# Performance work log

Hardware: AMD Instinct MI355X
Metric: run time of the kernel (lower is better)

The kernel has to match this reference:

```python
import jax, jax.numpy as jnp
import numpy as np

KH, KW = 3, 3
C_OUT = 32


def setup_inputs() -> dict:
    key = jax.random.key(0)
    k1, k2, k3 = jax.random.split(key, 3)
    B, H, W, C_IN = 32, 128, 128, 32
    P_DIM = 128
    X = jax.random.normal(k1, (B, H, W, C_IN), dtype=jnp.float32)
    P = jax.random.normal(k2, (B, P_DIM), dtype=jnp.float32)
    # hypernetwork Dense weight: p_dim -> kh*kw*c_in*c_out (no bias, no activation)
    dense_w = jax.random.normal(k3, (P_DIM, KH * KW * C_IN * C_OUT), dtype=jnp.float32) * 0.05
    return {"X": X, "P": P, "dense_w": dense_w}


def _conv_one(x, w):
    # x: [H, W, c_in], w: [kh, kw, c_in, c_out] -> [H, W, c_out], SAME padding, stride 1
    y = jax.lax.conv_general_dilated(
        x[None], w, window_strides=(1, 1), padding="SAME",
        dimension_numbers=("NHWC", "HWIO", "NHWC"))
    return y[0]


def reference(X, P, dense_w):
    B = X.shape[0]
    c_in = X.shape[-1]
    # hypernetwork: per-sample conv kernels
    A = P @ dense_w                              # [B, kh*kw*c_in*c_out]
    Wk = A.reshape(B, KH, KW, c_in, C_OUT)       # [B, kh, kw, c_in, c_out]
    # batched per-sample conv (equivalent to tf.map_fn over conv2d)
    return jax.vmap(_conv_one)(X, Wk)            # [B, H, W, c_out]
```

## Files before the change

### kernel.cpp

```cpp
#include <hip/hip_runtime.h>


#define BATCH 32
#define HDIM 128
#define WDIM 128
#define CIN 32
#define COUT 32
#define PDIM 128
#define KCOLS 9216

typedef _Float16 f16x8 __attribute__((ext_vector_type(8)));
typedef float f32x4 __attribute__((ext_vector_type(4)));

__device__ __forceinline__ f16x8 zero8() {
    f16x8 z;
#pragma unroll
    for (int j = 0; j < 8; ++j) z[j] = (_Float16)0.f;
    return z;
}

__device__ __forceinline__ f16x8 cvt8(f32x4 lo, f32x4 hi) {
    f16x8 o;
#pragma unroll
    for (int j = 0; j < 4; ++j) {
        o[j] = (_Float16)lo[j];
        o[4 + j] = (_Float16)hi[j];
    }
    return o;
}

__global__ __launch_bounds__(256) void hyper_gemm(const float* __restrict__ P,
                                                  const float* __restrict__ Dw,
                                                  unsigned short* __restrict__ WB) {
    const int tid = threadIdx.x;
    const int lane = tid & 63;
    const int cg = blockIdx.x % 144;
    const int bq = blockIdx.x / 144;
    const int col = cg * 64 + lane;
    const int b0 = __builtin_amdgcn_readfirstlane(bq * 16 + (tid >> 6) * 4);
    const float* pb = P + (size_t)b0 * PDIM;

    float acc[4];
#pragma unroll
    for (int j = 0; j < 4; ++j) acc[j] = 0.f;

#pragma unroll 2
    for (int mm = 0; mm < PDIM; mm += 16) {
        float d[16];
#pragma unroll
        for (int u = 0; u < 16; ++u) d[u] = Dw[(size_t)(mm + u) * KCOLS + col];
#pragma unroll
        for (int u = 0; u < 16; ++u) {
#pragma unroll
            for (int j = 0; j < 4; ++j) acc[j] += d[u] * pb[j * PDIM + mm + u];
        }
    }

    const int co = col & 31;
    const int k = col >> 5;
    const int kc = k >> 5;
    const int ci = k & 31;
    const int base =
        ((kc * 2 + (co >> 4)) * 64 + (ci >> 3) * 16 + (co & 15)) * 8 + (ci & 7);
#pragma unroll
    for (int j = 0; j < 4; ++j) {
        _Float16 v = (_Float16)acc[j];
        WB[(size_t)(b0 + j) * KCOLS + base] = __builtin_bit_cast(unsigned short, v);
    }
}

__device__ __forceinline__ f16x8 halo_ld(const f32x4* __restrict__ gp, int px) {
    const bool ok = (unsigned)px < 128u;
    const int p = ok ? px : 0;
    f32x4 lo = gp[p * 8];
    f32x4 hi = gp[p * 8 + 1];
    f16x8 o = cvt8(lo, hi);
    if (!ok) o = zero8();
    return o;
}

__global__ __launch_bounds__(256, 3) void conv_s4(const float* __restrict__ X,
                                                  const unsigned short* __restrict__ WB,
                                                  float* __restrict__ Y) {
    __shared__ f16x8 Xs[4 * 512];
    __shared__ f16x8 BFs[KCOLS / 8];
    const int tid = threadIdx.x;

    const int wg = blockIdx.x;
    const int id = (wg & 7) * 128 + (wg >> 3);
    const int b = id >> 5;
    const int hg = id & 31;
    const int r0 = hg * 4;

    const int wave = tid >> 6;
    const int lane = tid & 63;
    const int q = lane >> 4;
    const int m16 = lane & 15;

    {
        const f16x8* wbp = (const f16x8*)(WB + (size_t)b * KCOLS);
#pragma unroll
        for (int i = 0; i < 5; ++i) {
            const int idx = tid + i * 256;
            if (idx < KCOLS / 8) BFs[idx] = wbp[idx];
        }
    }

    {
        const int px_s = tid >> 1;
        const int qb = (tid & 1) * 2;
#pragma unroll
        for (int r = 0; r < 4; ++r) {
#pragma unroll
            for (int p = 0; p < 2; ++p) {
                const int q_s = qb + p;
                const float* src =
                    X + (((size_t)b * HDIM + r0 + r) * WDIM + px_s) * CIN + q_s * 8;
                f32x4 lo = *(const f32x4*)src;
                f32x4 hi = *(const f32x4*)(src + 4);
                const int g_s = px_s * 4 + ((q_s ^ (px_s >> 1)) & 3);
                Xs[r * 512 + g_s] = cvt8(lo, hi);
            }
        }
    }
    __syncthreads();

    const bool top = (wave == 0);
    const bool bot = (wave == 3);
    const bool gvalid = top ? (hg != 0) : (bot ? (hg != 31) : false);
    const int grow = top ? (hg ? r0 - 1 : 0) : (r0 + 4);
    const f32x4* gp = (const f32x4*)X +
                      ((size_t)b * HDIM + (gvalid ? grow : 0)) * (WDIM * CIN / 4) +
                      q * 2;

    f16x8 hal[3];
    if (gvalid) {
#pragma unroll
        for (int kw = 0; kw < 3; ++kw) hal[kw] = halo_ld(gp, m16 + kw - 1);
    } else {
#pragma unroll
        for (int kw = 0; kw < 3; ++kw) hal[kw] = zero8();
    }

    int va[3];
#pragma unroll
    for (int kw = 0; kw < 3; ++kw) {
        const int px = m16 + kw - 1;
        const int sl = (q ^ (px >> 1)) & 3;
        va[kw] = (wave - 1) * 8192 + px * 64 + sl * 16;
    }

    const char* xsb = (const char*)Xs;
    const f16x8* bfl = BFs + lane;
    const int h = r0 + wave;
    float* ybase = Y + (((size_t)b * HDIM + h) * WDIM + q * 4) * COUT + m16;

#pragma unroll
    for (int t = 0; t < 8; ++t) {
        f32x4 acc0 = {0.f, 0.f, 0.f, 0.f};
        f32x4 acc1 = {0.f, 0.f, 0.f, 0.f};

#pragma unroll
        for (int kh = 0; kh < 3; ++kh) {
            f16x8 a0, a1, a2;
            const bool use_lds =
                (kh == 1) || (kh == 0 && wave != 0) || (kh == 2 && wave != 3);
            if (use_lds) {
                int v0 = va[0] + kh * 8192;
                int v1 = va[1] + kh * 8192;
                int v2 = va[2] + kh * 8192;
                if (t == 0) v0 += (m16 == 0) ? 64 : 0;
                if (t == 7) v2 -= (m16 == 15) ? 64 : 0;
                a0 = *(const f16x8*)(xsb + v0);
                a1 = *(const f16x8*)(xsb + v1);
                a2 = *(const f16x8*)(xsb + v2);
                if (t == 0 && m16 == 0) a0 = zero8();
                if (t == 7 && m16 == 15) a2 = zero8();
            } else {
                a0 = hal[0];
                a1 = hal[1];
                a2 = hal[2];
                if (gvalid && t < 7) {
#pragma unroll
                    for (int kw = 0; kw < 3; ++kw)
                        hal[kw] = halo_ld(gp, (t + 1) * 16 + m16 + kw - 1);
                }
            }
            acc0 = __builtin_amdgcn_mfma_f32_16x16x32_f16(a0, bfl[((kh * 3 + 0) * 2 + 0) * 64], acc0, 0, 0, 0);
            acc1 = __builtin_amdgcn_mfma_f32_16x16x32_f16(a0, bfl[((kh * 3 + 0) * 2 + 1) * 64], acc1, 0, 0, 0);
            acc0 = __builtin_amdgcn_mfma_f32_16x16x32_f16(a1, bfl[((kh * 3 + 1) * 2 + 0) * 64], acc0, 0, 0, 0);
            acc1 = __builtin_amdgcn_mfma_f32_16x16x32_f16(a1, bfl[((kh * 3 + 1) * 2 + 1) * 64], acc1, 0, 0, 0);
            acc0 = __builtin_amdgcn_mfma_f32_16x16x32_f16(a2, bfl[((kh * 3 + 2) * 2 + 0) * 64], acc0, 0, 0, 0);
            acc1 = __builtin_amdgcn_mfma_f32_16x16x32_f16(a2, bfl[((kh * 3 + 2) * 2 + 1) * 64], acc1, 0, 0, 0);
        }

        float* yp = ybase + t * 16 * COUT;
#pragma unroll
        for (int r = 0; r < 4; ++r) {
            yp[r * COUT] = acc0[r];
            yp[r * COUT + 16] = acc1[r];
        }

#pragma unroll
        for (int kw = 0; kw < 3; ++kw) va[kw] += 1024;
    }
}

extern "C" void kernel_launch(void* const* d_in, const int* in_sizes, int n_in,
                              void* d_out, int out_size, void* d_ws, size_t ws_size,
                              hipStream_t stream) {
    const float* X = (const float*)d_in[0];
    const float* P = (const float*)d_in[1];
    const float* Dw = (const float*)d_in[2];
    float* Y = (float*)d_out;
    (void)ws_size;

    unsigned short* WB = (unsigned short*)d_ws;

    hipLaunchKernelGGL(hyper_gemm, dim3(288), dim3(256), 0, stream, P, Dw, WB);
    hipLaunchKernelGGL(conv_s4, dim3(1024), dim3(256), 0, stream, X, WB, Y);
}
```

Baseline: 146.7 us.

## Switch conv MFMA tiles from 16x16x32 to 32x32x16 with matching weight layout

Changes the per-wave conv tile from 16 pixels by 32 output channels, built from two 16x16x32 MFMAs, to a single 32x32x16 MFMA over 32 pixels and 32 output channels. The hypernetwork GEMM now writes weights in a layout that matches the new B-operand fragments, and the LDS and halo addressing are redone for 32-pixel tiles with two 8-channel halves. The aim is fewer MFMA issues and LDS B-fragment loads per output, at the cost of more live registers for halos and accumulators and a different store pattern.

Result: faster. 141.4 us (-3.6%).

```diff
diff --git a/kernel.cpp b/kernel.cpp
--- a/kernel.cpp
+++ b/kernel.cpp
@@ -11,6 +11,7 @@
 
 typedef _Float16 f16x8 __attribute__((ext_vector_type(8)));
 typedef float f32x4 __attribute__((ext_vector_type(4)));
+typedef float f32x16 __attribute__((ext_vector_type(16)));
 
 __device__ __forceinline__ f16x8 zero8() {
     f16x8 z;
@@ -61,7 +62,7 @@
     const int kc = k >> 5;
     const int ci = k & 31;
     const int base =
-        ((kc * 2 + (co >> 4)) * 64 + (ci >> 3) * 16 + (co & 15)) * 8 + (ci & 7);
+        ((kc * 2 + (ci >> 4)) * 64 + ((ci >> 3) & 1) * 32 + co) * 8 + (ci & 7);
 #pragma unroll
     for (int j = 0; j < 4; ++j) {
         _Float16 v = (_Float16)acc[j];
@@ -69,19 +70,20 @@
     }
 }
 
-__device__ __forceinline__ f16x8 halo_ld(const f32x4* __restrict__ gp, int px) {
+__device__ __forceinline__ f16x8 halo_ld32(const f32x4* __restrict__ gp, int px,
+                                           int oct) {
     const bool ok = (unsigned)px < 128u;
     const int p = ok ? px : 0;
-    f32x4 lo = gp[p * 8];
-    f32x4 hi = gp[p * 8 + 1];
+    f32x4 lo = gp[p * 8 + oct * 2];
+    f32x4 hi = gp[p * 8 + oct * 2 + 1];
     f16x8 o = cvt8(lo, hi);
     if (!ok) o = zero8();
     return o;
 }
 
-__global__ __launch_bounds__(256, 3) void conv_s4(const float* __restrict__ X,
-                                                  const unsigned short* __restrict__ WB,
-                                                  float* __restrict__ Y) {
+__global__ __launch_bounds__(256, 3) void conv_w32(const float* __restrict__ X,
+                                                   const unsigned short* __restrict__ WB,
+                                                   float* __restrict__ Y) {
     __shared__ f16x8 Xs[4 * 512];
     __shared__ f16x8 BFs[KCOLS / 8];
     const int tid = threadIdx.x;
@@ -94,8 +96,8 @@
 
     const int wave = tid >> 6;
     const int lane = tid & 63;
-    const int q = lane >> 4;
-    const int m16 = lane & 15;
+    const int m32 = lane & 31;
+    const int hi = lane >> 5;
 
     {
         const f16x8* wbp = (const f16x8*)(WB + (size_t)b * KCOLS);
@@ -117,9 +119,9 @@
                 const float* src =
                     X + (((size_t)b * HDIM + r0 + r) * WDIM + px_s) * CIN + q_s * 8;
                 f32x4 lo = *(const f32x4*)src;
-                f32x4 hi = *(const f32x4*)(src + 4);
+                f32x4 hi4 = *(const f32x4*)(src + 4);
                 const int g_s = px_s * 4 + ((q_s ^ (px_s >> 1)) & 3);
-                Xs[r * 512 + g_s] = cvt8(lo, hi);
+                Xs[r * 512 + g_s] = cvt8(lo, hi4);
             }
         }
     }
@@ -130,79 +132,98 @@
     const bool gvalid = top ? (hg != 0) : (bot ? (hg != 31) : false);
     const int grow = top ? (hg ? r0 - 1 : 0) : (r0 + 4);
     const f32x4* gp = (const f32x4*)X +
-                      ((size_t)b * HDIM + (gvalid ? grow : 0)) * (WDIM * CIN / 4) +
-                      q * 2;
-
-    f16x8 hal[3];
+                      ((size_t)b * HDIM + (gvalid ? grow : 0)) * (WDIM * CIN / 4);
+
+    f16x8 hal[3][2];
     if (gvalid) {
 #pragma unroll
-        for (int kw = 0; kw < 3; ++kw) hal[kw] = halo_ld(gp, m16 + kw - 1);
+        for (int kw = 0; kw < 3; ++kw)
+#pragma unroll
+            for (int h = 0; h < 2; ++h)
+                hal[kw][h] = halo_ld32(gp, m32 + kw - 1, 2 * h + hi);
     } else {
 #pragma unroll
-        for (int kw = 0; kw < 3; ++kw) hal[kw] = zero8();
-    }
-
-    int va[3];
-#pragma unroll
-    for (int kw = 0; kw < 3; ++kw) {
-        const int px = m16 + kw - 1;
-        const int sl = (q ^ (px >> 1)) & 3;
-        va[kw] = (wave - 1) * 8192 + px * 64 + sl * 16;
+        for (int kw = 0; kw < 3; ++kw)
+#pragma unroll
+            for (int h = 0; h < 2; ++h) hal[kw][h] = zero8();
+    }
+
+    int o0[2], o1[2], o2[2], o00[2];
+    {
+        const int p0 = m32 - 1, p1 = m32, p2 = m32 + 1;
+#pragma unroll
+        for (int h = 0; h < 2; ++h) {
+            const int s = 2 * h + hi;
+            o0[h] = p0 * 64 + ((s ^ ((p0 >> 1) & 3)) & 3) * 16;
+            o1[h] = p1 * 64 + ((s ^ ((p1 >> 1) & 3)) & 3) * 16;
+            o2[h] = p2 * 64 + ((s ^ ((p2 >> 1) & 3)) & 3) * 16;
+            const int pc = (m32 == 0) ? 0 : p0;
+            o00[h] = pc * 64 + ((s ^ ((pc >> 1) & 3)) & 3) * 16;
+        }
     }
 
     const char* xsb = (const char*)Xs;
     const f16x8* bfl = BFs + lane;
-    const int h = r0 + wave;
-    float* ybase = Y + (((size_t)b * HDIM + h) * WDIM + q * 4) * COUT + m16;
-
-#pragma unroll
-    for (int t = 0; t < 8; ++t) {
-        f32x4 acc0 = {0.f, 0.f, 0.f, 0.f};
-        f32x4 acc1 = {0.f, 0.f, 0.f, 0.f};
+    const int h_out = r0 + wave;
+    const int co = m32;
+    float* ybase = Y + (((size_t)b * HDIM + h_out) * WDIM) * COUT + co;
+
+#pragma unroll
+    for (int t = 0; t < 4; ++t) {
+        f32x16 acc = {};
 
 #pragma unroll
         for (int kh = 0; kh < 3; ++kh) {
-            f16x8 a0, a1, a2;
+            f16x8 a[3][2];
             const bool use_lds =
                 (kh == 1) || (kh == 0 && wave != 0) || (kh == 2 && wave != 3);
             if (use_lds) {
-                int v0 = va[0] + kh * 8192;
-                int v1 = va[1] + kh * 8192;
-                int v2 = va[2] + kh * 8192;
-                if (t == 0) v0 += (m16 == 0) ? 64 : 0;
-                if (t == 7) v2 -= (m16 == 15) ? 64 : 0;
-                a0 = *(const f16x8*)(xsb + v0);
-                a1 = *(const f16x8*)(xsb + v1);
-                a2 = *(const f16x8*)(xsb + v2);
-                if (t == 0 && m16 == 0) a0 = zero8();
-                if (t == 7 && m16 == 15) a2 = zero8();
+                const int ro = (wave - 1 + kh) * 8192;
+#pragma unroll
+                for (int h = 0; h < 2; ++h) {
+                    const int ad0 =
+                        ro + ((t == 0) ? o00[h] : (o0[h] + t * 2048));
+                    const int ad1 = ro + o1[h] + t * 2048;
+                    const int ad2 = ro + o2[h] + t * 2048 -
+                                    ((t == 3 && m32 == 31) ? 64 : 0);
+                    a[0][h] = *(const f16x8*)(xsb + ad0);
+                    a[1][h] = *(const f16x8*)(xsb + ad1);
+                    a[2][h] = *(const f16x8*)(xsb + ad2);
+                }
+                if (t == 0 && m32 == 0) { a[0][0] = zero8(); a[0][1] = zero8(); }
+                if (t == 3 && m32 == 31) { a[2][0] = zero8(); a[2][1] = zero8(); }
             } else {
-                a0 = hal[0];
-                a1 = hal[1];
-                a2 = hal[2];
-                if (gvalid && t < 7) {
+#pragma unroll
+                for (int kw = 0; kw < 3; ++kw)
+#pragma unroll
+                    for (int h = 0; h < 2; ++h) a[kw][h] = hal[kw][h];
+                if (gvalid && t < 3) {
 #pragma unroll
                     for (int kw = 0; kw < 3; ++kw)
-                        hal[kw] = halo_ld(gp, (t + 1) * 16 + m16 + kw - 1);
+#pragma unroll
+                        for (int h = 0; h < 2; ++h)
+                            hal[kw][h] = halo_ld32(gp, (t + 1) * 32 + m32 + kw - 1,
+                                                   2 * h + hi);
                 }
             }
-            acc0 = __builtin_amdgcn_mfma_f32_16x16x32_f16(a0, bfl[((kh * 3 + 0) * 2 + 0) * 64], acc0, 0, 0, 0);
-            acc1 = __builtin_amdgcn_mfma_f32_16x16x32_f16(a0, bfl[((kh * 3 + 0) * 2 + 1) * 64], acc1, 0, 0, 0);
-            acc0 = __builtin_amdgcn_mfma_f32_16x16x32_f16(a1, bfl[((kh * 3 + 1) * 2 + 0) * 64], acc0, 0, 0, 0);
-            acc1 = __builtin_amdgcn_mfma_f32_16x16x32_f16(a1, bfl[((kh * 3 + 1) * 2 + 1) * 64], acc1, 0, 0, 0);
-            acc0 = __builtin_amdgcn_mfma_f32_16x16x32_f16(a2, bfl[((kh * 3 + 2) * 2 + 0) * 64], acc0, 0, 0, 0);
-            acc1 = __builtin_amdgcn_mfma_f32_16x16x32_f16(a2, bfl[((kh * 3 + 2) * 2 + 1) * 64], acc1, 0, 0, 0);
-        }
-
-        float* yp = ybase + t * 16 * COUT;
-#pragma unroll
-        for (int r = 0; r < 4; ++r) {
-            yp[r * COUT] = acc0[r];
-            yp[r * COUT + 16] = acc1[r];
-        }
-
-#pragma unroll
-        for (int kw = 0; kw < 3; ++kw) va[kw] += 1024;
+#pragma unroll
+            for (int kw = 0; kw < 3; ++kw) {
+#pragma unroll
+                for (int h = 0; h < 2; ++h) {
+                    acc = __builtin_amdgcn_mfma_f32_32x32x16_f16(
+                        a[kw][h], bfl[(((kh * 3 + kw) * 2) + h) * 64], acc, 0, 0, 0);
+                }
+            }
+        }
+
+        float* yp = ybase + (size_t)(t * 32 + 4 * hi) * COUT;
+#pragma unroll
+        for (int r2 = 0; r2 < 4; ++r2) {
+#pragma unroll
+            for (int r1 = 0; r1 < 4; ++r1) {
+                yp[(size_t)(r1 + 8 * r2) * COUT] = acc[r2 * 4 + r1];
+            }
+        }
     }
 }
 
@@ -218,5 +239,5 @@
     unsigned short* WB = (unsigned short*)d_ws;
 
     hipLaunchKernelGGL(hyper_gemm, dim3(288), dim3(256), 0, stream, P, Dw, WB);
-    hipLaunchKernelGGL(conv_s4, dim3(1024), dim3(256), 0, stream, X, WB, Y);
-}
+    hipLaunchKernelGGL(conv_w32, dim3(1024), dim3(256), 0, stream, X, WB, Y);
+}
```

## Split conv work across 8 waves per block, two half-row waves per row

Applied to the files above, without the earlier changes.

Doubles the conv block to 512 threads, so each output row is handled by two waves that each cover half of the 8 column tiles. Staging loads are respread so each thread converts one 8-channel group per row. The aim is more waves in flight to hide LDS and global latency and to speed up the weight and input staging. The trade-off is more register and occupancy pressure under launch_bounds(512,8), and the halo loads for the top and bottom rows are now issued by two waves each.

Measured after the change: 139.7 us. -4.8%, faster.

```diff
diff --git a/kernel.cpp b/kernel.cpp
--- a/kernel.cpp
+++ b/kernel.cpp
@@ -79,9 +79,9 @@
     return o;
 }
 
-__global__ __launch_bounds__(256, 3) void conv_s4(const float* __restrict__ X,
-                                                  const unsigned short* __restrict__ WB,
-                                                  float* __restrict__ Y) {
+__global__ __launch_bounds__(512, 8) void conv_tlp(const float* __restrict__ X,
+                                                   const unsigned short* __restrict__ WB,
+                                                   float* __restrict__ Y) {
     __shared__ f16x8 Xs[4 * 512];
     __shared__ f16x8 BFs[KCOLS / 8];
     const int tid = threadIdx.x;
@@ -93,40 +93,35 @@
     const int r0 = hg * 4;
 
     const int wave = tid >> 6;
+    const int row = wave >> 1;
+    const int half = wave & 1;
     const int lane = tid & 63;
     const int q = lane >> 4;
     const int m16 = lane & 15;
+    const int t0 = half * 4;
 
     {
         const f16x8* wbp = (const f16x8*)(WB + (size_t)b * KCOLS);
-#pragma unroll
-        for (int i = 0; i < 5; ++i) {
-            const int idx = tid + i * 256;
-            if (idx < KCOLS / 8) BFs[idx] = wbp[idx];
-        }
+        for (int i = tid; i < KCOLS / 8; i += 512) BFs[i] = wbp[i];
     }
 
     {
-        const int px_s = tid >> 1;
-        const int qb = (tid & 1) * 2;
+        const int px_s = tid >> 2;
+        const int q_s = tid & 3;
+        const int g_s = px_s * 4 + ((q_s ^ (px_s >> 1)) & 3);
 #pragma unroll
         for (int r = 0; r < 4; ++r) {
-#pragma unroll
-            for (int p = 0; p < 2; ++p) {
-                const int q_s = qb + p;
-                const float* src =
-                    X + (((size_t)b * HDIM + r0 + r) * WDIM + px_s) * CIN + q_s * 8;
-                f32x4 lo = *(const f32x4*)src;
-                f32x4 hi = *(const f32x4*)(src + 4);
-                const int g_s = px_s * 4 + ((q_s ^ (px_s >> 1)) & 3);
-                Xs[r * 512 + g_s] = cvt8(lo, hi);
-            }
+            const float* src =
+                X + (((size_t)b * HDIM + r0 + r) * WDIM + px_s) * CIN + q_s * 8;
+            f32x4 lo = *(const f32x4*)src;
+            f32x4 hi = *(const f32x4*)(src + 4);
+            Xs[r * 512 + g_s] = cvt8(lo, hi);
         }
     }
     __syncthreads();
 
-    const bool top = (wave == 0);
-    const bool bot = (wave == 3);
+    const bool top = (row == 0);
+    const bool bot = (row == 3);
     const bool gvalid = top ? (hg != 0) : (bot ? (hg != 31) : false);
     const int grow = top ? (hg ? r0 - 1 : 0) : (r0 + 4);
     const f32x4* gp = (const f32x4*)X +
@@ -136,7 +131,8 @@
     f16x8 hal[3];
     if (gvalid) {
 #pragma unroll
-        for (int kw = 0; kw < 3; ++kw) hal[kw] = halo_ld(gp, m16 + kw - 1);
+        for (int kw = 0; kw < 3; ++kw)
+            hal[kw] = halo_ld(gp, t0 * 16 + m16 + kw - 1);
     } else {
 #pragma unroll
         for (int kw = 0; kw < 3; ++kw) hal[kw] = zero8();
@@ -145,18 +141,19 @@
     int va[3];
 #pragma unroll
     for (int kw = 0; kw < 3; ++kw) {
-        const int px = m16 + kw - 1;
+        const int px = t0 * 16 + m16 + kw - 1;
         const int sl = (q ^ (px >> 1)) & 3;
-        va[kw] = (wave - 1) * 8192 + px * 64 + sl * 16;
+        va[kw] = (row - 1) * 8192 + px * 64 + sl * 16;
     }
 
     const char* xsb = (const char*)Xs;
     const f16x8* bfl = BFs + lane;
-    const int h = r0 + wave;
+    const int h = r0 + row;
     float* ybase = Y + (((size_t)b * HDIM + h) * WDIM + q * 4) * COUT + m16;
 
 #pragma unroll
-    for (int t = 0; t < 8; ++t) {
+    for (int tt = 0; tt < 4; ++tt) {
+        const int t = t0 + tt;
         f32x4 acc0 = {0.f, 0.f, 0.f, 0.f};
         f32x4 acc1 = {0.f, 0.f, 0.f, 0.f};
 
@@ -164,23 +161,23 @@
         for (int kh = 0; kh < 3; ++kh) {
             f16x8 a0, a1, a2;
             const bool use_lds =
-                (kh == 1) || (kh == 0 && wave != 0) || (kh == 2 && wave != 3);
+                (kh == 1) || (kh == 0 && row != 0) || (kh == 2 && row != 3);
             if (use_lds) {
                 int v0 = va[0] + kh * 8192;
                 int v1 = va[1] + kh * 8192;
                 int v2 = va[2] + kh * 8192;
-                if (t == 0) v0 += (m16 == 0) ? 64 : 0;
-                if (t == 7) v2 -= (m16 == 15) ? 64 : 0;
+                if (half == 0 && tt == 0) v0 += (m16 == 0) ? 64 : 0;
+                if (half == 1 && tt == 3) v2 -= (m16 == 15) ? 64 : 0;
                 a0 = *(const f16x8*)(xsb + v0);
                 a1 = *(const f16x8*)(xsb + v1);
                 a2 = *(const f16x8*)(xsb + v2);
-                if (t == 0 && m16 == 0) a0 = zero8();
-                if (t == 7 && m16 == 15) a2 = zero8();
+                if (half == 0 && tt == 0 && m16 == 0) a0 = zero8();
+                if (half == 1 && tt == 3 && m16 == 15) a2 = zero8();
             } else {
                 a0 = hal[0];
                 a1 = hal[1];
                 a2 = hal[2];
-                if (gvalid && t < 7) {
+                if (gvalid && tt < 3) {
 #pragma unroll
                     for (int kw = 0; kw < 3; ++kw)
                         hal[kw] = halo_ld(gp, (t + 1) * 16 + m16 + kw - 1);
@@ -218,5 +215,5 @@
     unsigned short* WB = (unsigned short*)d_ws;
 
     hipLaunchKernelGGL(hyper_gemm, dim3(288), dim3(256), 0, stream, P, Dw, WB);
-    hipLaunchKernelGGL(conv_s4, dim3(1024), dim3(256), 0, stream, X, WB, Y);
-}
+    hipLaunchKernelGGL(conv_tlp, dim3(1024), dim3(512), 0, stream, X, WB, Y);
+}
```
